# Performance work log

Hardware: AMD Instinct MI355X
Metric: run time of the kernel (lower is better)

The kernel has to match this reference:

```python
import jax, jax.numpy as jnp
import numpy as np

POOLED_H = 7
POOLED_W = 7
SPATIAL_SCALE = 0.5


def _tent_integral(start, end, n):
    """Exact integral of the bilinear basis max(0, 1-|x-i|) over [start, end]
    for every integer grid point i in [0, n). start/end: [...]. Returns [..., n].
    This is the 1D factor of PrRoIPool's closed-form bilinear integral.
    """
    i = jnp.arange(n, dtype=start.dtype)
    a = jnp.clip(start[..., None] - i, -1.0, 1.0)
    b = jnp.clip(end[..., None] - i, -1.0, 1.0)

    def G(t):  # antiderivative of tent, with G(-1) = 0
        return jnp.where(t <= 0.0, 0.5 * (t + 1.0) ** 2, 1.0 - 0.5 * (1.0 - t) ** 2)

    return G(b) - G(a)


def setup_inputs() -> dict:
    key = jax.random.key(0)
    k1, k2, k3, k4 = jax.random.split(key, 4)
    N, C, H, W, R = 8, 256, 56, 56, 256
    features = jax.random.normal(k1, (N, C, H, W), dtype=jnp.float32)
    img_w, img_h = W / SPATIAL_SCALE, H / SPATIAL_SCALE
    bidx = jax.random.randint(k2, (R,), 0, N).astype(jnp.float32)
    xy1 = jax.random.uniform(k3, (R, 2)) * jnp.array([img_w * 0.7, img_h * 0.7], jnp.float32)
    wh = 8.0 + jax.random.uniform(k4, (R, 2)) * jnp.array([img_w * 0.3, img_h * 0.3], jnp.float32)
    rois = jnp.concatenate([bidx[:, None], xy1, xy1 + wh], axis=1)  # (b, x1, y1, x2, y2)
    return {"features": features, "rois": rois}


def reference(features, rois):
    """PrRoIPool2D(7, 7, spatial_scale=0.5): precise (integral) ROI pooling.

    out[r, c, ph, pw] = (1 / bin_area) * \int\int_bin bilinear(F[b_r, c], x, y) dx dy
    which factorizes as Iy^T F Ix with 1D tent-basis integrals.
    """
    N, C, H, W = features.shape
    dt = features.dtype
    batch = rois[:, 0].astype(jnp.int32)
    x1 = rois[:, 1] * SPATIAL_SCALE
    y1 = rois[:, 2] * SPATIAL_SCALE
    x2 = rois[:, 3] * SPATIAL_SCALE
    y2 = rois[:, 4] * SPATIAL_SCALE
    bw = (x2 - x1) / POOLED_W  # [R]
    bh = (y2 - y1) / POOLED_H

    pw = jnp.arange(POOLED_W, dtype=dt)
    ph = jnp.arange(POOLED_H, dtype=dt)
    xs = x1[:, None] + pw * bw[:, None]  # [R, 7] bin left edges
    ys = y1[:, None] + ph * bh[:, None]
    Ix = _tent_integral(xs, xs + bw[:, None], W)  # [R, 7, W]
    Iy = _tent_integral(ys, ys + bh[:, None], H)  # [R, 7, H]

    Fg = features[batch]  # [R, C, H, W] gather of shared map per ROI
    tmp = jnp.einsum('rchw,rqw->rchq', Fg, Ix)   # integrate over x
    acc = jnp.einsum('rph,rchq->rcpq', Iy, tmp)  # integrate over y -> [R, C, 7, 7]

    area = (bw * bh)[:, None, None, None]
    return jnp.where(area > 0.0, acc / jnp.maximum(area, jnp.asarray(1e-12, dt)), 0.0)
```

## Files before the change

kernel.cpp:

```cpp
#include <hip/hip_runtime.h>


#define POOLED 7
#define NHMAX 24
#define XS 9

__device__ __forceinline__ float Gfun(float t) {
    return (t <= 0.f) ? 0.5f * (t + 1.f) * (t + 1.f)
                      : 1.f - 0.5f * (1.f - t) * (1.f - t);
}
__device__ __forceinline__ float tent_int(float s, float e, float i) {
    float a = fminf(fmaxf(s - i, -1.f), 1.f);
    float b = fminf(fmaxf(e - i, -1.f), 1.f);
    return Gfun(b) - Gfun(a);
}

__global__ __launch_bounds__(256, 8)
void prroi_kernel(const float* __restrict__ F, const float* __restrict__ rois,
                  float* __restrict__ out, int C, int H, int W) {
    const int blk   = blockIdx.x;
    const int r     = blk >> 4;
    const int chunk = blk & 15;
    const int wave  = threadIdx.x >> 6;
    const int lane  = threadIdx.x & 63;

    __shared__ float s_wx[4][7][8];
    __shared__ float s_wy[4][7][6];
    __shared__ int   s_ox[4][8];
    __shared__ int   s_oy[4][8];
    __shared__ float s_xint[4][2][NHMAX][XS];

    const float* roi = rois + (size_t)r * 5;
    const int   b  = (int)roi[0];
    const float x1 = roi[1] * 0.5f, y1 = roi[2] * 0.5f;
    const float x2 = roi[3] * 0.5f, y2 = roi[4] * 0.5f;
    const float bw = (x2 - x1) * (1.f / POOLED);
    const float bh = (y2 - y1) * (1.f / POOLED);
    const float area = bw * bh;
    const float inv_area = (area > 0.f) ? 1.f / fmaxf(area, 1e-12f) : 0.f;

    if (lane < 7) {
        float s = x1 + lane * bw, e = s + bw;
        int o = ((int)ceilf(s - 1.f)) & ~3;
        o = min(max(o, 0), W - 8);
        s_ox[wave][lane] = o;
        #pragma unroll
        for (int k = 0; k < 8; ++k) s_wx[wave][lane][k] = tent_int(s, e, (float)(o + k));
    } else if (lane < 14) {
        int p = lane - 7;
        float s = y1 + p * bh, e = s + bh;
        int o = (int)ceilf(s - 1.f);
        o = min(max(o, 0), H - 6);
        s_oy[wave][p] = o;
        #pragma unroll
        for (int k = 0; k < 6; ++k) s_wy[wave][p][k] = tent_int(s, e, (float)(o + k)) * inv_area;
    }

    const int q1 = lane & 7, hs = lane >> 3;
    const bool a1 = (q1 < 7);
    const int qq = a1 ? q1 : 0;
    const int ox1 = s_ox[wave][qq];
    float wx1[8];
    #pragma unroll
    for (int k = 0; k < 8; ++k) wx1[k] = s_wx[wave][qq][k];

    const int p2 = lane >> 3, q2 = lane & 7;
    const bool a2 = (lane < 56) && (q2 < 7);
    const int pp = (p2 < 7) ? p2 : 0;
    const int hb  = s_oy[wave][0];
    const int nh  = s_oy[wave][6] + 6 - hb;
    const int yo2 = s_oy[wave][pp] - hb;
    float wy2[6];
    #pragma unroll
    for (int k = 0; k < 6; ++k) wy2[k] = s_wy[wave][pp][k];

    const int c0 = chunk * 16 + wave * 4;
    const float* Fb = F + ((size_t)b * C) * H * W;

    #pragma unroll
    for (int i = 0; i < 4; ++i) {
        const int c = c0 + i;
        const int buf = i & 1;
        const float* Fc = Fb + (size_t)c * H * W;

        #pragma unroll
        for (int it = 0; it < 3; ++it) {
            int hh = it * 8 + hs;
            if (a1 && hh < nh) {
                const float4* rp = (const float4*)(Fc + (hb + hh) * W + ox1);
                float4 v0 = rp[0], v1 = rp[1];
                float s = wx1[0] * v0.x + wx1[1] * v0.y + wx1[2] * v0.z + wx1[3] * v0.w
                        + wx1[4] * v1.x + wx1[5] * v1.y + wx1[6] * v1.z + wx1[7] * v1.w;
                s_xint[wave][buf][hh][q1] = s;
            }
        }
        if (a2) {
            float acc = 0.f;
            #pragma unroll
            for (int ky = 0; ky < 6; ++ky)
                acc += wy2[ky] * s_xint[wave][buf][yo2 + ky][q2];
            out[((size_t)r * C + c) * 49 + p2 * 7 + q2] = acc;
        }
    }
}

extern "C" void kernel_launch(void* const* d_in, const int* in_sizes, int n_in,
                              void* d_out, int out_size, void* d_ws, size_t ws_size,
                              hipStream_t stream) {
    const float* F    = (const float*)d_in[0];
    const float* rois = (const float*)d_in[1];
    float* out = (float*)d_out;

    const int C = 256, H = 56, W = 56;
    const int R = in_sizes[1] / 5;
    prroi_kernel<<<R * 16, 256, 0, stream>>>(F, rois, out, C, H, W);
}
```

Before: 84.40 us.

## Batch four channel row loads per wave and recompute offsets in registers

Restructures the per-wave loop so that each lane issues the row loads for all four channels together, with the row loop outermost and a runtime trip count. The x-integrals of all four channels go to four LDS buffers before the y-reduction runs. The weight setup is spread across all 64 lanes, and the x/y offsets are recomputed in registers instead of being held in shared memory. The aim is more memory-level parallelism and less serial load latency per wave, at the cost of more shared memory and registers, so occupancy drops to 6 waves per SIMD in the launch bounds.

```diff
diff --git a/kernel.cpp b/kernel.cpp
--- a/kernel.cpp
+++ b/kernel.cpp
@@ -15,7 +15,7 @@
     return Gfun(b) - Gfun(a);
 }
 
-__global__ __launch_bounds__(256, 8)
+__global__ __launch_bounds__(256, 6)
 void prroi_kernel(const float* __restrict__ F, const float* __restrict__ rois,
                   float* __restrict__ out, int C, int H, int W) {
     const int blk   = blockIdx.x;
@@ -26,9 +26,7 @@
 
     __shared__ float s_wx[4][7][8];
     __shared__ float s_wy[4][7][6];
-    __shared__ int   s_ox[4][8];
-    __shared__ int   s_oy[4][8];
-    __shared__ float s_xint[4][2][NHMAX][XS];
+    __shared__ float s_xint[4][4][NHMAX][XS];
 
     const float* roi = rois + (size_t)r * 5;
     const int   b  = (int)roi[0];
@@ -39,68 +37,66 @@
     const float area = bw * bh;
     const float inv_area = (area > 0.f) ? 1.f / fmaxf(area, 1e-12f) : 0.f;
 
-    if (lane < 7) {
-        float s = x1 + lane * bw, e = s + bw;
-        int o = ((int)ceilf(s - 1.f)) & ~3;
-        o = min(max(o, 0), W - 8);
-        s_ox[wave][lane] = o;
-        #pragma unroll
-        for (int k = 0; k < 8; ++k) s_wx[wave][lane][k] = tent_int(s, e, (float)(o + k));
-    } else if (lane < 14) {
-        int p = lane - 7;
-        float s = y1 + p * bh, e = s + bh;
-        int o = (int)ceilf(s - 1.f);
-        o = min(max(o, 0), H - 6);
-        s_oy[wave][p] = o;
-        #pragma unroll
-        for (int k = 0; k < 6; ++k) s_wy[wave][p][k] = tent_int(s, e, (float)(o + k)) * inv_area;
+    {
+        const int q = lane >> 3, k = lane & 7;
+        float sx = x1 + q * bw, ex = sx + bw;
+        int o = min(max(((int)ceilf(sx - 1.f)) & ~3, 0), W - 8);
+        float wv = tent_int(sx, ex, (float)(o + k));
+        if (q < 7) s_wx[wave][q][k] = wv;
+        float sy = y1 + q * bh, ey = sy + bh;
+        int oy = min(max((int)ceilf(sy - 1.f), 0), H - 6);
+        float wyv = tent_int(sy, ey, (float)(oy + k)) * inv_area;
+        if (q < 7 && k < 6) s_wy[wave][q][k] = wyv;
     }
 
     const int q1 = lane & 7, hs = lane >> 3;
-    const bool a1 = (q1 < 7);
-    const int qq = a1 ? q1 : 0;
-    const int ox1 = s_ox[wave][qq];
+    const int qq = min(q1, 6);
+    const int ox1 = min(max(((int)ceilf(x1 + qq * bw - 1.f)) & ~3, 0), W - 8);
     float wx1[8];
     #pragma unroll
     for (int k = 0; k < 8; ++k) wx1[k] = s_wx[wave][qq][k];
 
     const int p2 = lane >> 3, q2 = lane & 7;
-    const bool a2 = (lane < 56) && (q2 < 7);
-    const int pp = (p2 < 7) ? p2 : 0;
-    const int hb  = s_oy[wave][0];
-    const int nh  = s_oy[wave][6] + 6 - hb;
-    const int yo2 = s_oy[wave][pp] - hb;
+    const int pp = min(p2, 6);
+    const int hb  = min(max((int)ceilf(y1 - 1.f), 0), H - 6);
+    const int oy6 = min(max((int)ceilf(y1 + 6.f * bh - 1.f), 0), H - 6);
+    const int nh  = oy6 + 6 - hb;
+    const int yo2 = min(max((int)ceilf(y1 + pp * bh - 1.f), 0), H - 6) - hb;
     float wy2[6];
     #pragma unroll
     for (int k = 0; k < 6; ++k) wy2[k] = s_wy[wave][pp][k];
 
     const int c0 = chunk * 16 + wave * 4;
-    const float* Fb = F + ((size_t)b * C) * H * W;
+    const size_t HW = (size_t)H * W;
+    const float* Fc0 = F + ((size_t)b * C + c0) * HW;
 
-    #pragma unroll
-    for (int i = 0; i < 4; ++i) {
-        const int c = c0 + i;
-        const int buf = i & 1;
-        const float* Fc = Fb + (size_t)c * H * W;
-
-        #pragma unroll
-        for (int it = 0; it < 3; ++it) {
-            int hh = it * 8 + hs;
-            if (a1 && hh < nh) {
-                const float4* rp = (const float4*)(Fc + (hb + hh) * W + ox1);
+    const int itcnt = (nh + 7) >> 3;
+    for (int it = 0; it < itcnt; ++it) {
+        const int hh = it * 8 + hs;
+        if (hh < nh && q1 < 7) {
+            const float* rowb = Fc0 + (size_t)(hb + hh) * W + ox1;
+            #pragma unroll
+            for (int ch = 0; ch < 4; ++ch) {
+                const float4* rp = (const float4*)(rowb + ch * HW);
                 float4 v0 = rp[0], v1 = rp[1];
-                float s = wx1[0] * v0.x + wx1[1] * v0.y + wx1[2] * v0.z + wx1[3] * v0.w
-                        + wx1[4] * v1.x + wx1[5] * v1.y + wx1[6] * v1.z + wx1[7] * v1.w;
-                s_xint[wave][buf][hh][q1] = s;
+                float sA = wx1[0] * v0.x + wx1[1] * v0.y + wx1[2] * v0.z + wx1[3] * v0.w;
+                float sB = wx1[4] * v1.x + wx1[5] * v1.y + wx1[6] * v1.z + wx1[7] * v1.w;
+                s_xint[wave][ch][hh][q1] = sA + sB;
             }
         }
-        if (a2) {
-            float acc = 0.f;
-            #pragma unroll
-            for (int ky = 0; ky < 6; ++ky)
-                acc += wy2[ky] * s_xint[wave][buf][yo2 + ky][q2];
-            out[((size_t)r * C + c) * 49 + p2 * 7 + q2] = acc;
+    }
+
+    const bool st = (lane < 56) && (q2 < 7);
+    #pragma unroll
+    for (int ch = 0; ch < 4; ++ch) {
+        float aA = 0.f, aB = 0.f;
+        #pragma unroll
+        for (int ky = 0; ky < 6; ky += 2) {
+            aA += wy2[ky]     * s_xint[wave][ch][yo2 + ky][q2];
+            aB += wy2[ky + 1] * s_xint[wave][ch][yo2 + ky + 1][q2];
         }
+        if (st)
+            out[((size_t)r * C + c0 + ch) * 49 + p2 * 7 + q2] = aA + aB;
     }
 }
 
```

After: 80.99 us. 1.04x faster.
